# Performance work log

Hardware: AMD Instinct MI355X
Metric: run time of the kernel (lower is better)

Reference implementation:

```python
import jax, jax.numpy as jnp
import numpy as np
import math

EMBED_DIM = 128
NUM_HEADS = 16
HEAD_DIM = EMBED_DIM // NUM_HEADS  # = 8 = n_wires of the quantum circuit


def setup_inputs() -> dict:
    key = jax.random.key(0)
    k1, k2, k3 = jax.random.split(key, 3)
    B, S = 4, 2048
    x = jax.random.normal(k1, (B, S, EMBED_DIM), dtype=jnp.float32)
    # shared trainable RX angles of the single q_layer (applied to every head)
    theta = jax.random.normal(k2, (HEAD_DIM,), dtype=jnp.float32)
    w_out = jax.random.normal(k3, (EMBED_DIM, EMBED_DIM), dtype=jnp.float32) / math.sqrt(EMBED_DIM)
    mask = jnp.ones((B, S), dtype=jnp.int32)
    return {"x": x, "theta": theta, "w_out": w_out, "mask": mask}


def quantum_linear(x_head, theta):
    # Circuit: RX(x_i) encode + RX(theta_i) on wire i, CNOT chain (i, i+1),
    # then <Z_j>. For product state |psi_i> = RX(phi_i)|0>, <Z_i> = cos(phi_i),
    # and the CNOT chain gives final <Z_j> = prod_{i<=j} cos(phi_i).
    phi = x_head + theta  # [..., D] broadcast over leading dims
    return jnp.cumprod(jnp.cos(phi), axis=-1)


def reference(x, theta, w_out, mask):
    B, S, E = x.shape
    H, D = NUM_HEADS, HEAD_DIM
    xs = x.reshape(B, S, H, D)
    q = quantum_linear(xs, theta).transpose(0, 2, 1, 3)  # [B, H, S, D]; k = v = q
    scores = jnp.einsum("bhsd,bhtd->bhst", q, q) / math.sqrt(D)
    scores = jnp.where(mask[:, None, None, :] == 0, -1e9, scores)
    probs = jax.nn.softmax(scores, axis=-1)  # dropout is identity in eval
    attn = jnp.einsum("bhst,bhtd->bhsd", probs, q)
    attn = attn.transpose(0, 2, 1, 3).reshape(B, S, E)
    return attn @ w_out.T
```

## Files before the change

### kernel.cpp

```cpp
#include <hip/hip_runtime.h>
#include <hip/hip_bf16.h>
#include <hip/hip_fp16.h>

#define NB 4
#define NS 2048
#define NE 128
#define NH 16
#define ND 8

typedef __attribute__((ext_vector_type(8))) _Float16 half8;
typedef __attribute__((ext_vector_type(4))) float f32x4;

#define VSTRIDE  2056
#define VSTRIDEH 1032

__device__ __forceinline__ unsigned int pkrtz(float a, float b) {
    typedef __fp16 fp16v2 __attribute__((ext_vector_type(2)));
    union { fp16v2 h; unsigned int u; } v;
    v.h = __builtin_amdgcn_cvt_pkrtz(a, b);
    return v.u;
}
__device__ __forceinline__ unsigned short f2h(float a) {
    return __half_as_ushort(__float2half(a));
}
__device__ __forceinline__ half8 mk_half8(unsigned u0, unsigned u1,
                                          unsigned u2, unsigned u3) {
    union { half8 h; unsigned u[4]; } v;
    v.u[0] = u0; v.u[1] = u1; v.u[2] = u2; v.u[3] = u3;
    return v.h;
}
__device__ __forceinline__ void qrow(const float* xp, const float* th, float* p) {
    float4 a = *(const float4*)xp, c = *(const float4*)(xp + 4);
    float t = 1.f;
    t *= cosf(a.x + th[0]); p[0] = t; t *= cosf(a.y + th[1]); p[1] = t;
    t *= cosf(a.z + th[2]); p[2] = t; t *= cosf(a.w + th[3]); p[3] = t;
    t *= cosf(c.x + th[4]); p[4] = t; t *= cosf(c.y + th[5]); p[5] = t;
    t *= cosf(c.z + th[6]); p[6] = t; t *= cosf(c.w + th[7]); p[7] = t;
}

__global__ __launch_bounds__(512) void attn_partial(
        const float* __restrict__ x,
        const float* __restrict__ theta,
        const int* __restrict__ mask,
        float* __restrict__ Opart,
        float* __restrict__ lpart) {
    __shared__ unsigned short qt[1024 * ND + 24];
    __shared__ unsigned short vTh[9 * VSTRIDEH];
    __shared__ unsigned short qm[512 * ND + 8];

    const int bid = blockIdx.x;
    const int half = blockIdx.y;
    const int bh = bid >> 2;
    const int b = bh >> 4, h = bh & (NH - 1);
    const int mquart = bid & 3;
    const int tid = threadIdx.x;

    const float SC = 0.71421629f;

    float th[ND];
#pragma unroll
    for (int d = 0; d < ND; d++) th[d] = theta[d];

    {
        int m = mquart * 512 + tid;
        float pm[ND];
        qrow(x + ((size_t)(b * NS + m) * NE + h * ND), th, pm);
        uint4 qa;
        qa.x = pkrtz(pm[0] * SC, pm[1] * SC);
        qa.y = pkrtz(pm[2] * SC, pm[3] * SC);
        qa.z = pkrtz(pm[4] * SC, pm[5] * SC);
        qa.w = pkrtz(pm[6] * SC, pm[7] * SC);
        *(uint4*)&qm[tid * ND] = qa;
    }
    {
        int chs = tid >> 4, si = tid & 15;
        int ta = 4 * (si >> 2) + 2 * (si & 1) + 16 * ((si >> 1) & 1);
        int r0l = chs * 32 + ta;
        int t0 = half * 1024 + r0l, t1 = t0 + 1;
        float p0[ND], p1[ND];
        qrow(x + ((size_t)(b * NS + t0) * NE + h * ND), th, p0);
        qrow(x + ((size_t)(b * NS + t1) * NE + h * ND), th, p1);
        float sk0 = mask[b * NS + t0] ? SC : 0.f;
        float sk1 = mask[b * NS + t1] ? SC : 0.f;
        uint4 qa, qb;
        qa.x = pkrtz(p0[0] * SC, p0[1] * SC);
        qa.y = pkrtz(p0[2] * SC, p0[3] * SC);
        qa.z = pkrtz(p0[4] * SC, p0[5] * SC);
        qa.w = pkrtz(p0[6] * SC, p0[7] * SC);
        qb.x = pkrtz(p1[0] * SC, p1[1] * SC);
        qb.y = pkrtz(p1[2] * SC, p1[3] * SC);
        qb.z = pkrtz(p1[4] * SC, p1[5] * SC);
        qb.w = pkrtz(p1[6] * SC, p1[7] * SC);
        *(uint4*)&qt[r0l * ND]       = qa;
        *(uint4*)&qt[(r0l + 1) * ND] = qb;
#pragma unroll
        for (int d = 0; d < ND; d++)
            *(unsigned int*)&vTh[d * VSTRIDEH + chs * 32 + 2 * si] =
                pkrtz(p0[d] * sk0, p1[d] * sk1);
        *(unsigned int*)&vTh[8 * VSTRIDEH + chs * 32 + 2 * si] = pkrtz(sk0, sk1);
    }
    if (tid < 24) qt[1024 * ND + tid] = 0;
    __syncthreads();

    const int wave = tid >> 6, lane = tid & 63;
    const int quad = lane >> 4, l15 = lane & 15;
    const int vrow = (l15 < 9) ? l15 : 8;
    const unsigned short* vbase = &vTh[vrow * VSTRIDEH];
    half8 hz = {0, 0, 0, 0, 0, 0, 0, 0};

    half8 bm[4];
#pragma unroll
    for (int mt = 0; mt < 4; mt++)
        bm[mt] = quad ? hz : *(const half8*)&qm[(wave * 64 + mt * 16 + l15) * ND];

    f32x4 O[4] = {{0.f,0.f,0.f,0.f},{0.f,0.f,0.f,0.f},
                  {0.f,0.f,0.f,0.f},{0.f,0.f,0.f,0.f}};
    for (int ch = 0; ch < 32; ch++) {
        int tbl = ch * 32;
        half8 at0 = *(const half8*)&qt[(tbl + l15) * ND + quad * 8];
        half8 at1 = *(const half8*)&qt[(tbl + 16 + l15) * ND + quad * 8];
        half8 vf  = *(const half8*)&vbase[tbl + quad * 8];
        f32x4 z = {0.f, 0.f, 0.f, 0.f};

#pragma unroll
        for (int mt = 0; mt < 4; mt++) {
            f32x4 sa = __builtin_amdgcn_mfma_f32_16x16x32_f16(at0, bm[mt], z, 0, 0, 0);
            f32x4 sb = __builtin_amdgcn_mfma_f32_16x16x32_f16(at1, bm[mt], z, 0, 0, 0);
            half8 pA = mk_half8(
                pkrtz(__builtin_amdgcn_exp2f(sa[0]), __builtin_amdgcn_exp2f(sa[1])),
                pkrtz(__builtin_amdgcn_exp2f(sa[2]), __builtin_amdgcn_exp2f(sa[3])),
                pkrtz(__builtin_amdgcn_exp2f(sb[0]), __builtin_amdgcn_exp2f(sb[1])),
                pkrtz(__builtin_amdgcn_exp2f(sb[2]), __builtin_amdgcn_exp2f(sb[3])));
            O[mt] = __builtin_amdgcn_mfma_f32_16x16x32_f16(pA, vf, O[mt], 0, 0, 0);
        }
    }

    const int mbase = mquart * 512 + wave * 64;
    const size_t pb = ((size_t)half * 64 + bh) * NS;
#pragma unroll
    for (int mt = 0; mt < 4; mt++) {
#pragma unroll
        for (int r = 0; r < 4; r++) {
            int m = mbase + mt * 16 + quad * 4 + r;
            if (l15 < ND)
                Opart[(pb + m) * ND + l15] = O[mt][r];
            else if (l15 == ND)
                lpart[pb + m] = O[mt][r];
        }
    }
}

__global__ __launch_bounds__(256) void proj_combine(
        const float* __restrict__ Opart,
        const float* __restrict__ lpart,
        const float* __restrict__ w,
        float* __restrict__ out) {
    __shared__ unsigned short wf[NE * 136];
    __shared__ unsigned short am[32 * 136];
    const int rb = blockIdx.x * 32;
    const int tid = threadIdx.x;

    for (int i = tid; i < 2048; i += 256) {
        const float* wp = w + i * 8;
        float4 a = *(const float4*)wp, c = *(const float4*)(wp + 4);
        uint4 pk;
        pk.x = pkrtz(a.x, a.y); pk.y = pkrtz(a.z, a.w);
        pk.z = pkrtz(c.x, c.y); pk.w = pkrtz(c.z, c.w);
        int n = i >> 4, k8 = (i & 15) * 8;
        *(uint4*)&wf[n * 136 + k8] = pk;
    }
#pragma unroll
    for (int k = 0; k < 2; k++) {
        int c = k * 256 + tid;
        int r = c >> 4, h = c & 15;
        int R = rb + r, b = R >> 11, s = R & (NS - 1);
        size_t row = ((size_t)(b * NH + h)) * NS + s;
        size_t o0 = row * ND, o1 = o0 + (size_t)64 * NS * ND;
        float4 a0 = *(const float4*)&Opart[o0];
        float4 c0 = *(const float4*)&Opart[o0 + 4];
        float4 a1 = *(const float4*)&Opart[o1];
        float4 c1 = *(const float4*)&Opart[o1 + 4];
        float l = lpart[row] + lpart[(size_t)64 * NS + row];
        float inv = 1.f / l;
        uint4 pk;
        pk.x = pkrtz((a0.x + a1.x) * inv, (a0.y + a1.y) * inv);
        pk.y = pkrtz((a0.z + a1.z) * inv, (a0.w + a1.w) * inv);
        pk.z = pkrtz((c0.x + c1.x) * inv, (c0.y + c1.y) * inv);
        pk.w = pkrtz((c0.z + c1.z) * inv, (c0.w + c1.w) * inv);
        *(uint4*)&am[r * 136 + h * 8] = pk;
    }
    __syncthreads();

    const int wave = tid >> 6, lane = tid & 63;
    const int quad = lane >> 4, l15 = lane & 15;
    const int mt = wave & 1, nh = wave >> 1;

    half8 af[4];
#pragma unroll
    for (int kt = 0; kt < 4; kt++)
        af[kt] = *(const half8*)&am[(mt * 16 + l15) * 136 + kt * 32 + quad * 8];

#pragma unroll
    for (int nt = 0; nt < 4; nt++) {
        int n0 = (nh * 4 + nt) * 16;
        f32x4 acc = {0.f, 0.f, 0.f, 0.f};
#pragma unroll
        for (int kt = 0; kt < 4; kt++) {
            half8 bf = *(const half8*)&wf[(n0 + l15) * 136 + kt * 32 + quad * 8];
            acc = __builtin_amdgcn_mfma_f32_16x16x32_f16(af[kt], bf, acc, 0, 0, 0);
        }
#pragma unroll
        for (int r = 0; r < 4; r++)
            out[(size_t)(rb + mt * 16 + quad * 4 + r) * NE + n0 + l15] = acc[r];
    }
}

__global__ __launch_bounds__(512) void attn_full(
        const float* __restrict__ x,
        const float* __restrict__ theta,
        const int* __restrict__ mask,
        unsigned short* __restrict__ mid) {
    __shared__ unsigned short qhl[NS * ND + 24];
    __shared__ unsigned short vT[9 * VSTRIDE];
    __shared__ float kb[NS];

    const int bid = blockIdx.x;
    const int bh = bid >> 3;
    const int b = bh >> 4, h = bh & (NH - 1);
    const int meighth = bid & 7;
    const int tid = threadIdx.x;
    const float SC = 0.71421629f;

    float th[ND];
#pragma unroll
    for (int d = 0; d < ND; d++) th[d] = theta[d];

    for (int idx = tid; idx < 1024; idx += 512) {
        int chs = idx >> 4, si = idx & 15;
        int ta = 4 * (si >> 2) + 2 * (si & 1) + 16 * ((si >> 1) & 1);
        int r0 = chs * 32 + ta, r1 = r0 + 1;
        float p0[ND], p1[ND];
        qrow(x + ((size_t)(b * NS + r0) * NE + h * ND), th, p0);
        qrow(x + ((size_t)(b * NS + r1) * NE + h * ND), th, p1);
        uint4 qa, qb;
        qa.x = pkrtz(p0[0] * SC, p0[1] * SC);
        qa.y = pkrtz(p0[2] * SC, p0[3] * SC);
        qa.z = pkrtz(p0[4] * SC, p0[5] * SC);
        qa.w = pkrtz(p0[6] * SC, p0[7] * SC);
        qb.x = pkrtz(p1[0] * SC, p1[1] * SC);
        qb.y = pkrtz(p1[2] * SC, p1[3] * SC);
        qb.z = pkrtz(p1[4] * SC, p1[5] * SC);
        qb.w = pkrtz(p1[6] * SC, p1[7] * SC);
        *(uint4*)&qhl[r0 * ND] = qa;
        *(uint4*)&qhl[r1 * ND] = qb;
#pragma unroll
        for (int d = 0; d < ND; d++)
            *(unsigned int*)&vT[d * VSTRIDE + chs * 32 + 2 * si] = pkrtz(p0[d], p1[d]);
        *(unsigned int*)&vT[8 * VSTRIDE + chs * 32 + 2 * si] = 0x3C003C00u;
    }
    for (int i = tid; i < NS; i += 512)
        kb[i] = mask[b * NS + i] ? 0.f : -30000.f;
    if (tid < 24) qhl[NS * ND + tid] = 0;
    __syncthreads();

    const int wave = tid >> 6, lane = tid & 63;
    const int quad = lane >> 4, l15 = lane & 15;
    const int mbase = meighth * 256 + wave * 32;
    half8 hz = {0, 0, 0, 0, 0, 0, 0, 0};
    half8 bm0 = quad ? hz : *(const half8*)&qhl[(mbase + l15) * ND];
    half8 bm1 = quad ? hz : *(const half8*)&qhl[(mbase + 16 + l15) * ND];
    const int vrow = (l15 < 9) ? l15 : 8;
    const unsigned short* vbase = &vT[vrow * VSTRIDE];

    f32x4 O0 = {0.f, 0.f, 0.f, 0.f}, O1 = {0.f, 0.f, 0.f, 0.f};
    for (int ch = 0; ch < 64; ch++) {
        int tb = ch * 32;
        half8 at0 = *(const half8*)&qhl[(tb + l15) * ND + quad * 8];
        half8 at1 = *(const half8*)&qhl[(tb + 16 + l15) * ND + quad * 8];
        half8 vf  = *(const half8*)&vbase[tb + quad * 8];
        f32x4 C0 = *(const f32x4*)&kb[tb + quad * 4];
        f32x4 C1 = *(const f32x4*)&kb[tb + 16 + quad * 4];
        f32x4 s00 = __builtin_amdgcn_mfma_f32_16x16x32_f16(at0, bm0, C0, 0, 0, 0);
        f32x4 s01 = __builtin_amdgcn_mfma_f32_16x16x32_f16(at0, bm1, C0, 0, 0, 0);
        f32x4 s10 = __builtin_amdgcn_mfma_f32_16x16x32_f16(at1, bm0, C1, 0, 0, 0);
        f32x4 s11 = __builtin_amdgcn_mfma_f32_16x16x32_f16(at1, bm1, C1, 0, 0, 0);
        half8 pA0 = mk_half8(
            pkrtz(__builtin_amdgcn_exp2f(s00[0]), __builtin_amdgcn_exp2f(s00[1])),
            pkrtz(__builtin_amdgcn_exp2f(s00[2]), __builtin_amdgcn_exp2f(s00[3])),
            pkrtz(__builtin_amdgcn_exp2f(s10[0]), __builtin_amdgcn_exp2f(s10[1])),
            pkrtz(__builtin_amdgcn_exp2f(s10[2]), __builtin_amdgcn_exp2f(s10[3])));
        half8 pA1 = mk_half8(
            pkrtz(__builtin_amdgcn_exp2f(s01[0]), __builtin_amdgcn_exp2f(s01[1])),
            pkrtz(__builtin_amdgcn_exp2f(s01[2]), __builtin_amdgcn_exp2f(s01[3])),
            pkrtz(__builtin_amdgcn_exp2f(s11[0]), __builtin_amdgcn_exp2f(s11[1])),
            pkrtz(__builtin_amdgcn_exp2f(s11[2]), __builtin_amdgcn_exp2f(s11[3])));
        O0 = __builtin_amdgcn_mfma_f32_16x16x32_f16(pA0, vf, O0, 0, 0, 0);
        O1 = __builtin_amdgcn_mfma_f32_16x16x32_f16(pA1, vf, O1, 0, 0, 0);
    }
#pragma unroll
    for (int mt = 0; mt < 2; mt++) {
        f32x4 O = mt ? O1 : O0;
#pragma unroll
        for (int r = 0; r < 4; r++) {
            float lsum = __shfl(O[r], (lane & 48) | 8, 64);
            float v = O[r] / lsum;
            if (l15 < ND) {
                int m = mbase + mt * 16 + quad * 4 + r;
                mid[(size_t)(b * NS + m) * NE + h * ND + l15] = f2h(v);
            }
        }
    }
}

__global__ __launch_bounds__(256) void proj_mid(
        const unsigned short* __restrict__ mid,
        const float* __restrict__ w,
        float* __restrict__ out) {
    __shared__ unsigned short wf[NE * 136];
    __shared__ unsigned short am[32 * 136];
    const int rb = blockIdx.x * 32;
    const int tid = threadIdx.x;
    for (int i = tid; i < 2048; i += 256) {
        const float* wp = w + i * 8;
        float4 a = *(const float4*)wp, c = *(const float4*)(wp + 4);
        uint4 pk;
        pk.x = pkrtz(a.x, a.y); pk.y = pkrtz(a.z, a.w);
        pk.z = pkrtz(c.x, c.y); pk.w = pkrtz(c.z, c.w);
        int n = i >> 4, k8 = (i & 15) * 8;
        *(uint4*)&wf[n * 136 + k8] = pk;
    }
    for (int i = tid; i < 512; i += 256) {
        int r = i >> 4, k8 = (i & 15) * 8;
        uint4 v = *(const uint4*)&mid[(size_t)(rb + r) * NE + k8];
        *(uint4*)&am[r * 136 + k8] = v;
    }
    __syncthreads();
    const int wave = tid >> 6, lane = tid & 63;
    const int quad = lane >> 4, l15 = lane & 15;
    const int mt = wave & 1, nh = wave >> 1;
    half8 af[4];
#pragma unroll
    for (int kt = 0; kt < 4; kt++)
        af[kt] = *(const half8*)&am[(mt * 16 + l15) * 136 + kt * 32 + quad * 8];
#pragma unroll
    for (int nt = 0; nt < 4; nt++) {
        int n0 = (nh * 4 + nt) * 16;
        f32x4 acc = {0.f, 0.f, 0.f, 0.f};
#pragma unroll
        for (int kt = 0; kt < 4; kt++) {
            half8 bf = *(const half8*)&wf[(n0 + l15) * 136 + kt * 32 + quad * 8];
            acc = __builtin_amdgcn_mfma_f32_16x16x32_f16(af[kt], bf, acc, 0, 0, 0);
        }
#pragma unroll
        for (int r = 0; r < 4; r++)
            out[(size_t)(rb + mt * 16 + quad * 4 + r) * NE + n0 + l15] = acc[r];
    }
}

extern "C" void kernel_launch(void* const* d_in, const int* in_sizes, int n_in,
                              void* d_out, int out_size, void* d_ws, size_t ws_size,
                              hipStream_t stream) {
    const float* x     = (const float*)d_in[0];
    const float* theta = (const float*)d_in[1];
    const float* w_out = (const float*)d_in[2];
    const int*   mask  = (const int*)d_in[3];
    float* out = (float*)d_out;

    const size_t opart_elems = (size_t)2 * 64 * NS * ND;
    const size_t lpart_elems = (size_t)2 * 64 * NS;
    const size_t need = (opart_elems + lpart_elems) * sizeof(float);

    if (ws_size >= need) {
        float* Opart = (float*)d_ws;
        float* lpart = Opart + opart_elems;
        attn_partial<<<dim3(NB * NH * 4, 2), 512, 0, stream>>>(x, theta, mask, Opart, lpart);
        proj_combine<<<NB * NS / 32, 256, 0, stream>>>(Opart, lpart, w_out, out);
    } else {
        unsigned short* mid16 = (unsigned short*)d_ws;
        attn_full<<<NB * NH * 8, 512, 0, stream>>>(x, theta, mask, mid16);
        proj_mid<<<NB * NS / 32, 256, 0, stream>>>(mid16, w_out, out);
    }
}
```

Measured before the change: 103.4 us.

## Split keys into four partitions and use packed fp16 polynomial exp2

Key splitting goes from two partitions to four, doubling the grid so more workgroups run concurrently, and the combine kernel now sums four partial outputs and denominators. The per-element hardware exp2 calls plus conversion are replaced by a packed-half exp2 built from a cubic polynomial and exponent bit manipulation, meant to cut transcendental throughput cost. The trade-offs are more partial-result traffic and combine work, and lower exp accuracy with range limits in fp16.

```diff
diff --git a/kernel.cpp b/kernel.cpp
--- a/kernel.cpp
+++ b/kernel.cpp
@@ -10,9 +10,11 @@
 
 typedef __attribute__((ext_vector_type(8))) _Float16 half8;
 typedef __attribute__((ext_vector_type(4))) float f32x4;
+typedef __attribute__((ext_vector_type(2))) _Float16 h2v;
+typedef __attribute__((ext_vector_type(2))) unsigned short us2v;
 
 #define VSTRIDE  2056
-#define VSTRIDEH 1032
+#define VSTRIDEQ 520
 
 __device__ __forceinline__ unsigned int pkrtz(float a, float b) {
     typedef __fp16 fp16v2 __attribute__((ext_vector_type(2)));
@@ -28,6 +30,25 @@
     union { half8 h; unsigned u[4]; } v;
     v.u[0] = u0; v.u[1] = u1; v.u[2] = u2; v.u[3] = u3;
     return v.h;
+}
+__device__ __forceinline__ unsigned exp2pk(unsigned su) {
+    union { unsigned u; h2v h; us2v s; } X, T, B, R;
+    X.u = su;
+    const h2v M  = {(_Float16)1536.0f, (_Float16)1536.0f};
+    const h2v c3 = {(_Float16)0.0555041f, (_Float16)0.0555041f};
+    const h2v c2 = {(_Float16)0.2402265f, (_Float16)0.2402265f};
+    const h2v c1 = {(_Float16)0.6931472f, (_Float16)0.6931472f};
+    const h2v c0 = {(_Float16)1.0f, (_Float16)1.0f};
+    h2v t  = X.h + M;
+    h2v nf = t - M;
+    h2v f  = X.h - nf;
+    h2v p  = ((f * c3 + c2) * f + c1) * f + c0;
+    T.h = t;
+    const us2v mg = {0x65F1, 0x65F1};
+    const us2v sh = {10, 10};
+    B.s = (us2v)((T.s - mg) << sh);
+    R.h = p * B.h;
+    return R.u;
 }
 __device__ __forceinline__ void qrow(const float* xp, const float* th, float* p) {
     float4 a = *(const float4*)xp, c = *(const float4*)(xp + 4);
@@ -44,12 +65,12 @@
         const int* __restrict__ mask,
         float* __restrict__ Opart,
         float* __restrict__ lpart) {
-    __shared__ unsigned short qt[1024 * ND + 24];
-    __shared__ unsigned short vTh[9 * VSTRIDEH];
+    __shared__ unsigned short qt[512 * ND + 24];
+    __shared__ unsigned short vTq[9 * VSTRIDEQ];
     __shared__ unsigned short qm[512 * ND + 8];
 
     const int bid = blockIdx.x;
-    const int half = blockIdx.y;
+    const int qtr = blockIdx.y;
     const int bh = bid >> 2;
     const int b = bh >> 4, h = bh & (NH - 1);
     const int mquart = bid & 3;
@@ -72,11 +93,11 @@
         qa.w = pkrtz(pm[6] * SC, pm[7] * SC);
         *(uint4*)&qm[tid * ND] = qa;
     }
-    {
+    if (tid < 256) {
         int chs = tid >> 4, si = tid & 15;
         int ta = 4 * (si >> 2) + 2 * (si & 1) + 16 * ((si >> 1) & 1);
         int r0l = chs * 32 + ta;
-        int t0 = half * 1024 + r0l, t1 = t0 + 1;
+        int t0 = qtr * 512 + r0l, t1 = t0 + 1;
         float p0[ND], p1[ND];
         qrow(x + ((size_t)(b * NS + t0) * NE + h * ND), th, p0);
         qrow(x + ((size_t)(b * NS + t1) * NE + h * ND), th, p1);
@@ -95,17 +116,17 @@
         *(uint4*)&qt[(r0l + 1) * ND] = qb;
 #pragma unroll
         for (int d = 0; d < ND; d++)
-            *(unsigned int*)&vTh[d * VSTRIDEH + chs * 32 + 2 * si] =
+            *(unsigned int*)&vTq[d * VSTRIDEQ + chs * 32 + 2 * si] =
                 pkrtz(p0[d] * sk0, p1[d] * sk1);
-        *(unsigned int*)&vTh[8 * VSTRIDEH + chs * 32 + 2 * si] = pkrtz(sk0, sk1);
-    }
-    if (tid < 24) qt[1024 * ND + tid] = 0;
+        *(unsigned int*)&vTq[8 * VSTRIDEQ + chs * 32 + 2 * si] = pkrtz(sk0, sk1);
+    }
+    if (tid < 24) qt[512 * ND + tid] = 0;
     __syncthreads();
 
     const int wave = tid >> 6, lane = tid & 63;
     const int quad = lane >> 4, l15 = lane & 15;
     const int vrow = (l15 < 9) ? l15 : 8;
-    const unsigned short* vbase = &vTh[vrow * VSTRIDEH];
+    const unsigned short* vbase = &vTq[vrow * VSTRIDEQ];
     half8 hz = {0, 0, 0, 0, 0, 0, 0, 0};
 
     half8 bm[4];
@@ -115,7 +136,7 @@
 
     f32x4 O[4] = {{0.f,0.f,0.f,0.f},{0.f,0.f,0.f,0.f},
                   {0.f,0.f,0.f,0.f},{0.f,0.f,0.f,0.f}};
-    for (int ch = 0; ch < 32; ch++) {
+    for (int ch = 0; ch < 16; ch++) {
         int tbl = ch * 32;
         half8 at0 = *(const half8*)&qt[(tbl + l15) * ND + quad * 8];
         half8 at1 = *(const half8*)&qt[(tbl + 16 + l15) * ND + quad * 8];
@@ -127,16 +148,16 @@
             f32x4 sa = __builtin_amdgcn_mfma_f32_16x16x32_f16(at0, bm[mt], z, 0, 0, 0);
             f32x4 sb = __builtin_amdgcn_mfma_f32_16x16x32_f16(at1, bm[mt], z, 0, 0, 0);
             half8 pA = mk_half8(
-                pkrtz(__builtin_amdgcn_exp2f(sa[0]), __builtin_amdgcn_exp2f(sa[1])),
-                pkrtz(__builtin_amdgcn_exp2f(sa[2]), __builtin_amdgcn_exp2f(sa[3])),
-                pkrtz(__builtin_amdgcn_exp2f(sb[0]), __builtin_amdgcn_exp2f(sb[1])),
-                pkrtz(__builtin_amdgcn_exp2f(sb[2]), __builtin_amdgcn_exp2f(sb[3])));
+                exp2pk(pkrtz(sa[0], sa[1])),
+                exp2pk(pkrtz(sa[2], sa[3])),
+                exp2pk(pkrtz(sb[0], sb[1])),
+                exp2pk(pkrtz(sb[2], sb[3])));
             O[mt] = __builtin_amdgcn_mfma_f32_16x16x32_f16(pA, vf, O[mt], 0, 0, 0);
         }
     }
 
     const int mbase = mquart * 512 + wave * 64;
-    const size_t pb = ((size_t)half * 64 + bh) * NS;
+    const size_t pb = ((size_t)qtr * 64 + bh) * NS;
 #pragma unroll
     for (int mt = 0; mt < 4; mt++) {
 #pragma unroll
@@ -175,18 +196,23 @@
         int r = c >> 4, h = c & 15;
         int R = rb + r, b = R >> 11, s = R & (NS - 1);
         size_t row = ((size_t)(b * NH + h)) * NS + s;
-        size_t o0 = row * ND, o1 = o0 + (size_t)64 * NS * ND;
-        float4 a0 = *(const float4*)&Opart[o0];
-        float4 c0 = *(const float4*)&Opart[o0 + 4];
-        float4 a1 = *(const float4*)&Opart[o1];
-        float4 c1 = *(const float4*)&Opart[o1 + 4];
-        float l = lpart[row] + lpart[(size_t)64 * NS + row];
+        float o[ND] = {0,0,0,0,0,0,0,0};
+        float l = 0.f;
+#pragma unroll
+        for (int q = 0; q < 4; q++) {
+            size_t ro = ((size_t)q * 64 * NS + row);
+            float4 a0 = *(const float4*)&Opart[ro * ND];
+            float4 c0 = *(const float4*)&Opart[ro * ND + 4];
+            o[0] += a0.x; o[1] += a0.y; o[2] += a0.z; o[3] += a0.w;
+            o[4] += c0.x; o[5] += c0.y; o[6] += c0.z; o[7] += c0.w;
+            l += lpart[ro];
+        }
         float inv = 1.f / l;
         uint4 pk;
-        pk.x = pkrtz((a0.x + a1.x) * inv, (a0.y + a1.y) * inv);
-        pk.y = pkrtz((a0.z + a1.z) * inv, (a0.w + a1.w) * inv);
-        pk.z = pkrtz((c0.x + c1.x) * inv, (c0.y + c1.y) * inv);
-        pk.w = pkrtz((c0.z + c1.z) * inv, (c0.w + c1.w) * inv);
+        pk.x = pkrtz(o[0] * inv, o[1] * inv);
+        pk.y = pkrtz(o[2] * inv, o[3] * inv);
+        pk.z = pkrtz(o[4] * inv, o[5] * inv);
+        pk.w = pkrtz(o[6] * inv, o[7] * inv);
         *(uint4*)&am[r * 136 + h * 8] = pk;
     }
     __syncthreads();
@@ -366,14 +392,14 @@
     const int*   mask  = (const int*)d_in[3];
     float* out = (float*)d_out;
 
-    const size_t opart_elems = (size_t)2 * 64 * NS * ND;
-    const size_t lpart_elems = (size_t)2 * 64 * NS;
+    const size_t opart_elems = (size_t)4 * 64 * NS * ND;
+    const size_t lpart_elems = (size_t)4 * 64 * NS;
     const size_t need = (opart_elems + lpart_elems) * sizeof(float);
 
     if (ws_size >= need) {
         float* Opart = (float*)d_ws;
         float* lpart = Opart + opart_elems;
-        attn_partial<<<dim3(NB * NH * 4, 2), 512, 0, stream>>>(x, theta, mask, Opart, lpart);
+        attn_partial<<<dim3(NB * NH * 4, 4), 512, 0, stream>>>(x, theta, mask, Opart, lpart);
         proj_combine<<<NB * NS / 32, 256, 0, stream>>>(Opart, lpart, w_out, out);
     } else {
         unsigned short* mid16 = (unsigned short*)d_ws;
```

New measurement: 125.8 us. 21.7% more time.
